# Performance work log

Measured on AMD Instinct MI355X. Metric: run time of the kernel, lower is better.

## Reference

```python
import jax, jax.numpy as jnp
import numpy as np


def quantize_uniform(x, n_bits, clip):
    # clamp to [-clip, clip], round to 2^(1-n_bits)*clip grid, cap at clip*(1-b)
    b = 2.0 ** (1 - n_bits)
    xc = jnp.clip(x, -clip, clip)
    return clip * jnp.minimum(b * jnp.round(xc / (b * clip)), 1.0 - b)


def quantize_act(x, n_bits, clip):
    # clip to [0, clip], round to 2^-n_bits grid, cap at 1 - 2^-n_bits
    s = 2.0 ** n_bits
    xc = jnp.clip(x, 0.0, clip)
    return jnp.minimum(jnp.round(xc * s) / s, 1.0 - 1.0 / s)


def qconv(x, w, b, pad):
    # fake-quantized conv: weights/bias quant(8,1), input quant(8,4), output quant(8,8)
    wq = quantize_uniform(w, 8, 1.0)
    bq = quantize_uniform(b, 8, 1.0)
    xq = quantize_uniform(x, 8, 4.0)
    y = jax.lax.conv_general_dilated(
        xq, wq, window_strides=(1, 1), padding=[(pad, pad), (pad, pad)],
        dimension_numbers=('NCHW', 'OIHW', 'NCHW'))
    y = y + bq[None, :, None, None]
    return quantize_uniform(y, 8, 8.0)


def setup_inputs() -> dict:
    key = jax.random.key(0)
    ks = jax.random.split(key, 7)
    N, Cin, H, W = 32, 128, 56, 56
    Sq, E1, E3 = 32, 128, 128
    x = jax.random.normal(ks[0], (N, Cin, H, W), dtype=jnp.float32)
    w_sq = jax.random.normal(ks[1], (Sq, Cin, 1, 1), dtype=jnp.float32) * 0.05
    b_sq = jax.random.normal(ks[2], (Sq,), dtype=jnp.float32) * 0.05
    w_e1 = jax.random.normal(ks[3], (E1, Sq, 1, 1), dtype=jnp.float32) * 0.05
    b_e1 = jax.random.normal(ks[4], (E1,), dtype=jnp.float32) * 0.05
    w_e3 = jax.random.normal(ks[5], (E3, Sq, 3, 3), dtype=jnp.float32) * 0.05
    b_e3 = jax.random.normal(ks[6], (E3,), dtype=jnp.float32) * 0.05
    return {'x': x, 'w_sq': w_sq, 'b_sq': b_sq, 'w_e1': w_e1, 'b_e1': b_e1,
            'w_e3': w_e3, 'b_e3': b_e3}


def reference(x, w_sq, b_sq, w_e1, b_e1, w_e3, b_e3):
    h = jax.nn.relu(qconv(x, w_sq, b_sq, pad=0))
    h = quantize_act(h, 13, 4.0)
    y1 = jax.nn.relu(qconv(h, w_e1, b_e1, pad=0))
    y3 = jax.nn.relu(qconv(h, w_e3, b_e3, pad=1))
    return jnp.concatenate([y1, y3], axis=1)
```

## Files before the change

kernel.cpp:

```cpp
#include <hip/hip_runtime.h>
#include <stdint.h>

typedef __bf16 bf16x8 __attribute__((ext_vector_type(8)));
typedef float  f32x4  __attribute__((ext_vector_type(4)));

#define HW   3136
#define WID  56
#define CIN  128
#define SQ   32

#define OFF_BSQ 0
#define OFF_BE  32
#define WSQF_BYTES_OFF 1152
#define WE1F_BYTES_OFF 9344
#define WE3F_BYTES_OFF 17536

__device__ __forceinline__ float quant_w8(float x){
  float xc = fminf(fmaxf(x,-1.f),1.f);
  return fminf(rintf(xc*128.f)*0.0078125f, 0.9921875f);
}
__device__ __forceinline__ ushort wq_int_bf16(float x){
  float xc = fminf(fmaxf(x,-1.f),1.f);
  float n = fminf(rintf(xc*128.f), 127.f);
  return (ushort)(__float_as_uint(n)>>16);
}
__device__ __forceinline__ uint pack2f(float a, float b){
  return (__float_as_uint(a)>>16) | (__float_as_uint(b)&0xffff0000u);
}

__global__ void prep_kernel(const float* __restrict__ wsq, const float* __restrict__ bsq,
                            const float* __restrict__ we1, const float* __restrict__ be1,
                            const float* __restrict__ we3, const float* __restrict__ be3,
                            float* __restrict__ ws){
  int tid = blockIdx.x*blockDim.x+threadIdx.x;
  int nth = gridDim.x*blockDim.x;
  ushort* wsqf = (ushort*)((char*)ws + WSQF_BYTES_OFF);
  ushort* we1f = (ushort*)((char*)ws + WE1F_BYTES_OFF);
  ushort* we3f = (ushort*)((char*)ws + WE3F_BYTES_OFF);
  for (int i=tid;i<SQ;i+=nth) ws[OFF_BSQ+i]=quant_w8(bsq[i]);
  for (int i=tid;i<256;i+=nth) ws[OFF_BE+i] = (i<128)? quant_w8(be1[i]) : quant_w8(be3[i-128]);
  for (int i=tid;i<4096;i+=nth){
    int mfkc=i>>9, l=(i>>3)&63, j=i&7;
    int mf=mfkc>>2, kc=mfkc&3;
    int co=mf*16+(l&15), ci=kc*32+(l>>4)*8+j;
    wsqf[i] = wq_int_bf16(wsq[co*CIN+ci]);
  }
  for (int i=tid;i<4096;i+=nth){
    int mf=i>>9, l=(i>>3)&63, j=i&7;
    int co=mf*16+(l&15), ci=(l>>4)*8+j;
    we1f[i] = wq_int_bf16(we1[co*SQ+ci]);
  }
  for (int i=tid;i<36864;i+=nth){
    int mf=i/4608, r=i-mf*4608, t=r>>9, l=(r>>3)&63, j=r&7;
    int co=mf*16+(l&15), ci=(l>>4)*8+j;
    we3f[i] = wq_int_bf16(we3[(co*SQ+ci)*9+t]);
  }
}

__global__ __launch_bounds__(256, 4) void fire_kernel(const float* __restrict__ x,
    const float* __restrict__ ws, float* __restrict__ out){
  __shared__ uint4 lds4[928];
  int bry = blockIdx.x;
  int n   = blockIdx.y;
  int tid = threadIdx.x, w = tid>>6, lane = tid&63;
  int colg = lane&15, kg = lane>>4;
  int R0 = bry*2;
  int vr0 = (R0==0) ? 0 : R0-1;
  int vr1 = (R0+2 > 55) ? 55 : R0+2;
  int limit = (vr1+1)*WID;
  int nblk = ((vr1-vr0+1)*WID + 15)>>4;
  int base_px = vr0*WID;

  uint4 z = make_uint4(0,0,0,0);
  for (int i=tid; i<928; i+=256) lds4[i] = z;
  __syncthreads();

  {
    const bf16x8* wsqf = (const bf16x8*)((const char*)ws + WSQF_BYTES_OFF);
    bf16x8 W[8];
    #pragma unroll
    for (int q=0;q<8;++q) W[q] = wsqf[q*64 + lane];
    float bias[2][4];
    #pragma unroll
    for (int mf=0;mf<2;++mf)
      #pragma unroll
      for (int r=0;r<4;++r) bias[mf][r] = ws[OFF_BSQ + mf*16 + kg*4 + r];

    for (int b=w; b<nblk; b+=4){
      int px = base_px + b*16 + colg;
      int pxc = (px < limit) ? px : (limit-1);
      const float* xp = x + (size_t)n*CIN*HW + pxc;
      float xv[32];
      #pragma unroll
      for (int kc=0;kc<4;++kc)
        #pragma unroll
        for (int j=0;j<8;++j)
          xv[kc*8+j] = xp[(size_t)(kc*32 + kg*8 + j)*HW];

      bf16x8 Bf[4];
      #pragma unroll
      for (int kc=0;kc<4;++kc){
        float m[8];
        #pragma unroll
        for (int j=0;j<8;++j){
          float v = fminf(fmaxf(xv[kc*8+j],-4.f),4.f);
          m[j] = fminf(rintf(v*32.f), 127.f);
        }
        union { uint u[4]; bf16x8 v; } cv;
        #pragma unroll
        for (int q=0;q<4;++q) cv.u[q] = pack2f(m[q*2], m[q*2+1]);
        Bf[kc] = cv.v;
      }

      f32x4 acc0 = (f32x4){0.f,0.f,0.f,0.f};
      f32x4 acc1 = (f32x4){0.f,0.f,0.f,0.f};
      #pragma unroll
      for (int kc=0;kc<4;++kc){
        acc0 = __builtin_amdgcn_mfma_f32_16x16x32_bf16(W[kc],   Bf[kc], acc0, 0,0,0);
        acc1 = __builtin_amdgcn_mfma_f32_16x16x32_bf16(W[4+kc], Bf[kc], acc1, 0,0,0);
      }

      if (px < limit){
        int rr = px/WID, c = px - rr*WID;
        int ph = (rr - R0 + 1)*58 + c + 1;
        #pragma unroll
        for (int mf=0;mf<2;++mf){
          f32x4 a = mf ? acc1 : acc0;
          float m[4];
          #pragma unroll
          for (int r=0;r<4;++r){
            float y = fmaf(a[r], 0.000244140625f, bias[mf][r]);
            y = fminf(fmaxf(y,-8.f),8.f);
            y = fminf(rintf(y*16.f)*0.0625f, 7.9375f);
            y = fmaxf(y,0.f);
            y = fminf(y,4.f);
            y = fminf(y,0.9998779296875f);
            m[r] = rintf(y*32.f);
          }
          int chunk = mf*2 + (kg>>1);
          int idx = ph*4 + (chunk ^ ((ph>>1)&3));
          uint* dst = (uint*)&lds4[idx] + (kg&1)*2;
          dst[0] = pack2f(m[0], m[1]);
          dst[1] = pack2f(m[2], m[3]);
        }
      }
    }
  }
  __syncthreads();

  int wid = w;
  const bf16x8* we1f = (const bf16x8*)((const char*)ws + WE1F_BYTES_OFF);
  const bf16x8* we3f = (const bf16x8*)((const char*)ws + WE3F_BYTES_OFF);
  const bf16x8* lbase = (const bf16x8*)lds4;

  int baseh[7];
  #pragma unroll
  for (int nf=0;nf<7;++nf){
    int p = nf*16 + colg;
    int rr = p/WID, c = p - rr*WID;
    baseh[nf] = (rr+1)*58 + c + 1;
  }

  f32x4 acc[4][7];
  #pragma unroll
  for (int mi=0;mi<4;++mi)
    #pragma unroll
    for (int nf=0;nf<7;++nf)
      acc[mi][nf] = (f32x4){0.f,0.f,0.f,0.f};

  #pragma unroll
  for (int t=0;t<9;++t){
    int off = (t/3 - 1)*58 + (t%3 - 1);
    bf16x8 B[7];
    #pragma unroll
    for (int nf=0;nf<7;++nf){
      int ph = baseh[nf] + off;
      int idx = ph*4 + (kg ^ ((ph>>1)&3));
      B[nf] = lbase[idx];
    }
    bf16x8 A2 = we3f[(wid*9+t)*64 + lane];
    bf16x8 A3 = we3f[((wid+4)*9+t)*64 + lane];
    #pragma unroll
    for (int nf=0;nf<7;++nf){
      acc[2][nf] = __builtin_amdgcn_mfma_f32_16x16x32_bf16(B[nf], A2, acc[2][nf], 0,0,0);
      acc[3][nf] = __builtin_amdgcn_mfma_f32_16x16x32_bf16(B[nf], A3, acc[3][nf], 0,0,0);
    }
    if (t==4){
      bf16x8 A0 = we1f[wid*64 + lane];
      bf16x8 A1 = we1f[(wid+4)*64 + lane];
      #pragma unroll
      for (int nf=0;nf<7;++nf){
        acc[0][nf] = __builtin_amdgcn_mfma_f32_16x16x32_bf16(B[nf], A0, acc[0][nf], 0,0,0);
        acc[1][nf] = __builtin_amdgcn_mfma_f32_16x16x32_bf16(B[nf], A1, acc[1][nf], 0,0,0);
      }
    }
  }

  #pragma unroll
  for (int mi=0;mi<4;++mi){
    int co = (wid+mi*4)*16 + colg;
    float bias = ws[OFF_BE + co];
    float* opb = out + (size_t)(n*256+co)*HW + R0*WID + kg*4;
    #pragma unroll
    for (int nf=0;nf<7;++nf){
      f32x4 a = acc[mi][nf];
      f32x4 yv;
      #pragma unroll
      for (int r=0;r<4;++r){
        float y = fmaf(a[r], 0.000244140625f, bias);
        y = fminf(fmaxf(y,-8.f),8.f);
        y = fminf(rintf(y*16.f)*0.0625f, 7.9375f);
        y = fmaxf(y,0.f);
        yv[r] = y;
      }
      *(f32x4*)(opb + nf*16) = yv;
    }
  }
}

extern "C" void kernel_launch(void* const* d_in, const int* in_sizes, int n_in,
                              void* d_out, int out_size, void* d_ws, size_t ws_size,
                              hipStream_t stream){
  const float* x   = (const float*)d_in[0];
  const float* wsq = (const float*)d_in[1];
  const float* bsq = (const float*)d_in[2];
  const float* we1 = (const float*)d_in[3];
  const float* be1 = (const float*)d_in[4];
  const float* we3 = (const float*)d_in[5];
  const float* be3 = (const float*)d_in[6];
  float* out = (float*)d_out;
  float* ws  = (float*)d_ws;

  hipLaunchKernelGGL(prep_kernel, dim3(64), dim3(256), 0, stream,
                     wsq, bsq, we1, be1, we3, be3, ws);
  hipLaunchKernelGGL(fire_kernel, dim3(28, 32), dim3(256), 0, stream, x, ws, out);
}
```

Baseline: 51.63 us.

## Process four output rows per block and double-buffer squeeze input loads

Each block now covers four output rows instead of two, so the squeeze conv's halo rows are recomputed less and less input is reread. The expand phase runs in two sub-tiles to keep accumulator registers bounded. Input loads in the squeeze loop are software-pipelined with two register buffers to overlap global loads with MFMA work. The grid is halved and occupancy bounds are relaxed, which reduces parallelism and latency hiding.

```diff
diff --git a/kernel.cpp b/kernel.cpp
--- a/kernel.cpp
+++ b/kernel.cpp
@@ -57,22 +57,80 @@
   }
 }
 
-__global__ __launch_bounds__(256, 4) void fire_kernel(const float* __restrict__ x,
+#define LOADX(dst, b) { \
+  int px_ = base_px + (b)*16 + colg; \
+  int pxc_ = (px_ < limit) ? px_ : (limit-1); \
+  const float* xp_ = xb + pxc_; \
+  _Pragma("unroll") \
+  for (int kc_=0;kc_<4;++kc_) \
+    _Pragma("unroll") \
+    for (int j_=0;j_<8;++j_) \
+      dst[kc_*8+j_] = xp_[(size_t)(kc_*32 + kg*8 + j_)*HW]; }
+
+#define PROCX(src, b) { \
+  bf16x8 Bf_[4]; \
+  _Pragma("unroll") \
+  for (int kc_=0;kc_<4;++kc_){ \
+    float m_[8]; \
+    _Pragma("unroll") \
+    for (int j_=0;j_<8;++j_){ \
+      float v_ = fminf(fmaxf(src[kc_*8+j_],-4.f),4.f); \
+      m_[j_] = fminf(rintf(v_*32.f), 127.f); \
+    } \
+    union { uint u[4]; bf16x8 v; } cv_; \
+    _Pragma("unroll") \
+    for (int q_=0;q_<4;++q_) cv_.u[q_] = pack2f(m_[q_*2], m_[q_*2+1]); \
+    Bf_[kc_] = cv_.v; \
+  } \
+  f32x4 a0_ = (f32x4){0.f,0.f,0.f,0.f}; \
+  f32x4 a1_ = (f32x4){0.f,0.f,0.f,0.f}; \
+  _Pragma("unroll") \
+  for (int kc_=0;kc_<4;++kc_){ \
+    a0_ = __builtin_amdgcn_mfma_f32_16x16x32_bf16(W[kc_],   Bf_[kc_], a0_, 0,0,0); \
+    a1_ = __builtin_amdgcn_mfma_f32_16x16x32_bf16(W[4+kc_], Bf_[kc_], a1_, 0,0,0); \
+  } \
+  int px_ = base_px + (b)*16 + colg; \
+  if (px_ < limit){ \
+    int rr_ = px_/WID, c_ = px_ - rr_*WID; \
+    int ph_ = (rr_ - R0 + 1)*58 + c_ + 1; \
+    _Pragma("unroll") \
+    for (int mf_=0;mf_<2;++mf_){ \
+      f32x4 a_ = mf_ ? a1_ : a0_; \
+      float m_[4]; \
+      _Pragma("unroll") \
+      for (int r_=0;r_<4;++r_){ \
+        float y_ = fmaf(a_[r_], 0.000244140625f, bias[mf_][r_]); \
+        y_ = fminf(fmaxf(y_,-8.f),8.f); \
+        y_ = fminf(rintf(y_*16.f)*0.0625f, 7.9375f); \
+        y_ = fmaxf(y_,0.f); \
+        y_ = fminf(y_,4.f); \
+        y_ = fminf(y_,0.9998779296875f); \
+        m_[r_] = rintf(y_*32.f); \
+      } \
+      int chunk_ = mf_*2 + (kg>>1); \
+      int idx_ = ph_*4 + (chunk_ ^ ((ph_>>1)&3)); \
+      uint* dst_ = (uint*)&lds4[idx_] + (kg&1)*2; \
+      dst_[0] = pack2f(m_[0], m_[1]); \
+      dst_[1] = pack2f(m_[2], m_[3]); \
+    } \
+  } }
+
+__global__ __launch_bounds__(256, 2) void fire_kernel(const float* __restrict__ x,
     const float* __restrict__ ws, float* __restrict__ out){
-  __shared__ uint4 lds4[928];
+  __shared__ uint4 lds4[1392];
   int bry = blockIdx.x;
   int n   = blockIdx.y;
   int tid = threadIdx.x, w = tid>>6, lane = tid&63;
   int colg = lane&15, kg = lane>>4;
-  int R0 = bry*2;
+  int R0 = bry*4;
   int vr0 = (R0==0) ? 0 : R0-1;
-  int vr1 = (R0+2 > 55) ? 55 : R0+2;
+  int vr1 = (R0+4 > 55) ? 55 : R0+4;
   int limit = (vr1+1)*WID;
   int nblk = ((vr1-vr0+1)*WID + 15)>>4;
   int base_px = vr0*WID;
 
   uint4 z = make_uint4(0,0,0,0);
-  for (int i=tid; i<928; i+=256) lds4[i] = z;
+  for (int i=tid; i<1392; i+=256) lds4[i] = z;
   __syncthreads();
 
   {
@@ -86,63 +144,23 @@
       #pragma unroll
       for (int r=0;r<4;++r) bias[mf][r] = ws[OFF_BSQ + mf*16 + kg*4 + r];
 
-    for (int b=w; b<nblk; b+=4){
-      int px = base_px + b*16 + colg;
-      int pxc = (px < limit) ? px : (limit-1);
-      const float* xp = x + (size_t)n*CIN*HW + pxc;
-      float xv[32];
-      #pragma unroll
-      for (int kc=0;kc<4;++kc)
-        #pragma unroll
-        for (int j=0;j<8;++j)
-          xv[kc*8+j] = xp[(size_t)(kc*32 + kg*8 + j)*HW];
-
-      bf16x8 Bf[4];
-      #pragma unroll
-      for (int kc=0;kc<4;++kc){
-        float m[8];
-        #pragma unroll
-        for (int j=0;j<8;++j){
-          float v = fminf(fmaxf(xv[kc*8+j],-4.f),4.f);
-          m[j] = fminf(rintf(v*32.f), 127.f);
-        }
-        union { uint u[4]; bf16x8 v; } cv;
-        #pragma unroll
-        for (int q=0;q<4;++q) cv.u[q] = pack2f(m[q*2], m[q*2+1]);
-        Bf[kc] = cv.v;
-      }
-
-      f32x4 acc0 = (f32x4){0.f,0.f,0.f,0.f};
-      f32x4 acc1 = (f32x4){0.f,0.f,0.f,0.f};
-      #pragma unroll
-      for (int kc=0;kc<4;++kc){
-        acc0 = __builtin_amdgcn_mfma_f32_16x16x32_bf16(W[kc],   Bf[kc], acc0, 0,0,0);
-        acc1 = __builtin_amdgcn_mfma_f32_16x16x32_bf16(W[4+kc], Bf[kc], acc1, 0,0,0);
-      }
-
-      if (px < limit){
-        int rr = px/WID, c = px - rr*WID;
-        int ph = (rr - R0 + 1)*58 + c + 1;
-        #pragma unroll
-        for (int mf=0;mf<2;++mf){
-          f32x4 a = mf ? acc1 : acc0;
-          float m[4];
-          #pragma unroll
-          for (int r=0;r<4;++r){
-            float y = fmaf(a[r], 0.000244140625f, bias[mf][r]);
-            y = fminf(fmaxf(y,-8.f),8.f);
-            y = fminf(rintf(y*16.f)*0.0625f, 7.9375f);
-            y = fmaxf(y,0.f);
-            y = fminf(y,4.f);
-            y = fminf(y,0.9998779296875f);
-            m[r] = rintf(y*32.f);
-          }
-          int chunk = mf*2 + (kg>>1);
-          int idx = ph*4 + (chunk ^ ((ph>>1)&3));
-          uint* dst = (uint*)&lds4[idx] + (kg&1)*2;
-          dst[0] = pack2f(m[0], m[1]);
-          dst[1] = pack2f(m[2], m[3]);
-        }
+    const float* xb = x + (size_t)n*CIN*HW;
+    float xvA[32], xvB[32];
+    int b = w;
+    if (b < nblk){
+      LOADX(xvA, b);
+      while (true){
+        int b2 = b + 4;
+        if (b2 < nblk){
+          LOADX(xvB, b2);
+          PROCX(xvA, b);
+          int b3 = b2 + 4;
+          if (b3 < nblk){
+            LOADX(xvA, b3);
+            PROCX(xvB, b2);
+            b = b3;
+          } else { PROCX(xvB, b2); break; }
+        } else { PROCX(xvA, b); break; }
       }
     }
   }
@@ -153,67 +171,73 @@
   const bf16x8* we3f = (const bf16x8*)((const char*)ws + WE3F_BYTES_OFF);
   const bf16x8* lbase = (const bf16x8*)lds4;
 
-  int baseh[7];
+  float biasv[4];
   #pragma unroll
-  for (int nf=0;nf<7;++nf){
-    int p = nf*16 + colg;
-    int rr = p/WID, c = p - rr*WID;
-    baseh[nf] = (rr+1)*58 + c + 1;
-  }
-
-  f32x4 acc[4][7];
+  for (int mi=0;mi<4;++mi) biasv[mi] = ws[OFF_BE + (wid+mi*4)*16 + colg];
+
   #pragma unroll
-  for (int mi=0;mi<4;++mi)
-    #pragma unroll
-    for (int nf=0;nf<7;++nf)
-      acc[mi][nf] = (f32x4){0.f,0.f,0.f,0.f};
-
-  #pragma unroll
-  for (int t=0;t<9;++t){
-    int off = (t/3 - 1)*58 + (t%3 - 1);
-    bf16x8 B[7];
+  for (int s=0; s<2; ++s){
+    int baseh[7];
     #pragma unroll
     for (int nf=0;nf<7;++nf){
-      int ph = baseh[nf] + off;
-      int idx = ph*4 + (kg ^ ((ph>>1)&3));
-      B[nf] = lbase[idx];
-    }
-    bf16x8 A2 = we3f[(wid*9+t)*64 + lane];
-    bf16x8 A3 = we3f[((wid+4)*9+t)*64 + lane];
-    #pragma unroll
-    for (int nf=0;nf<7;++nf){
-      acc[2][nf] = __builtin_amdgcn_mfma_f32_16x16x32_bf16(B[nf], A2, acc[2][nf], 0,0,0);
-      acc[3][nf] = __builtin_amdgcn_mfma_f32_16x16x32_bf16(B[nf], A3, acc[3][nf], 0,0,0);
-    }
-    if (t==4){
-      bf16x8 A0 = we1f[wid*64 + lane];
-      bf16x8 A1 = we1f[(wid+4)*64 + lane];
+      int p = s*112 + nf*16 + colg;
+      int rr = p/WID, c = p - rr*WID;
+      baseh[nf] = (rr+1)*58 + c + 1;
+    }
+
+    f32x4 acc[4][7];
+    #pragma unroll
+    for (int mi=0;mi<4;++mi)
+      #pragma unroll
+      for (int nf=0;nf<7;++nf)
+        acc[mi][nf] = (f32x4){0.f,0.f,0.f,0.f};
+
+    #pragma unroll
+    for (int t=0;t<9;++t){
+      int off = (t/3 - 1)*58 + (t%3 - 1);
+      bf16x8 B[7];
       #pragma unroll
       for (int nf=0;nf<7;++nf){
-        acc[0][nf] = __builtin_amdgcn_mfma_f32_16x16x32_bf16(B[nf], A0, acc[0][nf], 0,0,0);
-        acc[1][nf] = __builtin_amdgcn_mfma_f32_16x16x32_bf16(B[nf], A1, acc[1][nf], 0,0,0);
-      }
-    }
-  }
-
-  #pragma unroll
-  for (int mi=0;mi<4;++mi){
-    int co = (wid+mi*4)*16 + colg;
-    float bias = ws[OFF_BE + co];
-    float* opb = out + (size_t)(n*256+co)*HW + R0*WID + kg*4;
-    #pragma unroll
-    for (int nf=0;nf<7;++nf){
-      f32x4 a = acc[mi][nf];
-      f32x4 yv;
-      #pragma unroll
-      for (int r=0;r<4;++r){
-        float y = fmaf(a[r], 0.000244140625f, bias);
-        y = fminf(fmaxf(y,-8.f),8.f);
-        y = fminf(rintf(y*16.f)*0.0625f, 7.9375f);
-        y = fmaxf(y,0.f);
-        yv[r] = y;
-      }
-      *(f32x4*)(opb + nf*16) = yv;
+        int ph = baseh[nf] + off;
+        int idx = ph*4 + (kg ^ ((ph>>1)&3));
+        B[nf] = lbase[idx];
+      }
+      bf16x8 A2 = we3f[(wid*9+t)*64 + lane];
+      bf16x8 A3 = we3f[((wid+4)*9+t)*64 + lane];
+      #pragma unroll
+      for (int nf=0;nf<7;++nf){
+        acc[2][nf] = __builtin_amdgcn_mfma_f32_16x16x32_bf16(B[nf], A2, acc[2][nf], 0,0,0);
+        acc[3][nf] = __builtin_amdgcn_mfma_f32_16x16x32_bf16(B[nf], A3, acc[3][nf], 0,0,0);
+      }
+      if (t==4){
+        bf16x8 A0 = we1f[wid*64 + lane];
+        bf16x8 A1 = we1f[(wid+4)*64 + lane];
+        #pragma unroll
+        for (int nf=0;nf<7;++nf){
+          acc[0][nf] = __builtin_amdgcn_mfma_f32_16x16x32_bf16(B[nf], A0, acc[0][nf], 0,0,0);
+          acc[1][nf] = __builtin_amdgcn_mfma_f32_16x16x32_bf16(B[nf], A1, acc[1][nf], 0,0,0);
+        }
+      }
+    }
+
+    #pragma unroll
+    for (int mi=0;mi<4;++mi){
+      int co = (wid+mi*4)*16 + colg;
+      float* opb = out + (size_t)(n*256+co)*HW + R0*WID + s*112 + kg*4;
+      #pragma unroll
+      for (int nf=0;nf<7;++nf){
+        f32x4 a = acc[mi][nf];
+        f32x4 yv;
+        #pragma unroll
+        for (int r=0;r<4;++r){
+          float y = fmaf(a[r], 0.000244140625f, biasv[mi]);
+          y = fminf(fmaxf(y,-8.f),8.f);
+          y = fminf(rintf(y*16.f)*0.0625f, 7.9375f);
+          y = fmaxf(y,0.f);
+          yv[r] = y;
+        }
+        *(f32x4*)(opb + nf*16) = yv;
+      }
     }
   }
 }
@@ -233,5 +257,5 @@
 
   hipLaunchKernelGGL(prep_kernel, dim3(64), dim3(256), 0, stream,
                      wsq, bsq, we1, be1, we3, be3, ws);
-  hipLaunchKernelGGL(fire_kernel, dim3(28, 32), dim3(256), 0, stream, x, ws, out);
-}
+  hipLaunchKernelGGL(fire_kernel, dim3(14, 32), dim3(256), 0, stream, x, ws, out);
+}
```

After: 44.99 us. -12.9%, faster.
